# Kernel optimization log

Measured on AMD Instinct MI355X. Metric: run time of the kernel, lower is better.

## Reference

```python
import jax, jax.numpy as jnp
import numpy as np

B, T, E, H = 8, 1024, 768, 12  # batch, num_tokens, embed_dim (=dk=dv), num_heads


def setup_inputs() -> dict:
    key = jax.random.key(0)
    ks = jax.random.split(key, 5)
    return {
        "x": jax.random.normal(ks[0], (B, T, E), dtype=jnp.float32),
        "WQ": jax.random.normal(ks[1], (H, E, E), dtype=jnp.float32),
        "WK": jax.random.normal(ks[2], (H, E, E), dtype=jnp.float32),
        "WV": jax.random.normal(ks[3], (H, E, E), dtype=jnp.float32),
        "WO": jax.random.normal(ks[4], (H * E, E), dtype=jnp.float32),
    }


def reference(x, WQ, WK, WV, WO):
    b, t, e = x.shape
    h = WQ.shape[0]
    dk = WQ.shape[2]
    dv = WV.shape[2]
    # Batched QKV projections for all heads at once: (h, b, t, d)
    Q = jnp.einsum('bte,hek->hbtk', x, WQ)
    K = jnp.einsum('bte,hek->hbtk', x, WK)
    V = jnp.einsum('bte,hev->hbtv', x, WV)
    # Faithful quirk: original does K.view(b, e, t) -- a row-major RESHAPE,
    # not a transpose (valid because dk == e).
    K_rs = K.reshape(h, b, e, t)
    scores = jnp.matmul(Q, K_rs)  # (h, b, t, t)
    # Faithful quirks: scale by sqrt(num_tokens) (K.size(1) == t), and
    # Softmax(1) normalizes over the QUERY axis (axis 1 of (b,t,t) -> axis -2).
    A = jax.nn.softmax(scores / jnp.sqrt(jnp.asarray(t, scores.dtype)), axis=-2)
    Z = jnp.matmul(A, V)  # (h, b, t, dv)
    # Original: Z[bb] has layout (h, t, dv); reshape(t, h*dv) flat in row-major.
    Zc = jnp.transpose(Z, (1, 0, 2, 3)).reshape(b, h, t, dv)
    Zc = Zc.reshape(b, h * t * dv).reshape(b, t, h * dv)  # row-major flat of (h,t,dv)
    return jnp.matmul(Zc, WO)  # (b, t, e)
```

## Files before the change

kernel.cpp:

```cpp
#include <hip/hip_runtime.h>


typedef __bf16 bf16x8 __attribute__((ext_vector_type(8)));
typedef float  f32x4  __attribute__((ext_vector_type(4)));
typedef unsigned short u16;
typedef u16 u16x8 __attribute__((ext_vector_type(8)));
typedef u16 u16x4 __attribute__((ext_vector_type(4)));
typedef unsigned int u32;

#define RC 16

__device__ __forceinline__ float bf2f(u16 u) {
    union { u32 i; float f; } x; x.i = ((u32)u) << 16; return x.f;
}
__device__ __forceinline__ u16 f2bf(float f) {
    __bf16 h = (__bf16)f; union { __bf16 b; u16 u; } x; x.b = h; return x.u;
}
__device__ __forceinline__ void split2(float v, u16& h, u16& l) {
    h = f2bf(v); l = f2bf(v - bf2f(h));
}

__device__ __forceinline__ void gl16(const void* g, void* l) {
    __builtin_amdgcn_global_load_lds(
        (const __attribute__((address_space(1))) u32*)g,
        (__attribute__((address_space(3))) u32*)l, 16, 0, 0);
}

template<int BKMAJ, int WIN>
__device__ __forceinline__ void core(
    const u16* __restrict__ Ah, const u16* __restrict__ Al,
    const u16* __restrict__ Bh, const u16* __restrict__ Bl,
    float* __restrict__ C, u16* __restrict__ Ch, u16* __restrict__ Cl,
    int K, int lda, int ldb, int ldc,
    long long aShift, long long aHi, const u16* __restrict__ zp,
    int mClip, int mode, int mtile, int kChunk, int kChunks, int n0)
{
    __shared__ u16 Ahs[4096], Als[4096], Bhs[4096], Bls[4096];

    const int tid = threadIdx.x, lane = tid & 63, w = tid >> 6;
    const int m0 = mtile * 128;
    const int wm = (w & 1) << 6, wn = (w >> 1) << 6;
    const int lr = lane & 15, lq = lane >> 4;
    const int rs = (lr >> 1) & 3;
    const int fro = (lq ^ rs) << 4;

    const int srow = (w << 4) + (lane >> 2);
    const int kk = (((lane & 3) ^ ((srow >> 1) & 3)) << 3);
    const int lds0 = (w << 10), lds1 = lds0 + 4096;

    const int nB = tid & 127, khB = (tid >> 7) << 4;
    const int rsB = (nB >> 1) & 3;
    const int sB0 = (((khB >> 3) ^ rsB) << 4);
    const int sB1 = ((((khB >> 3) | 1) ^ rsB) << 4);

    f32x4 acc[4][4] = {};
    const int kLen = K / kChunks;
    const int kBeg = kChunk * kLen, kEnd = kBeg + kLen;

    u16 rBh[16], rBl[16];
    auto loadB = [&](int k0) {
        if constexpr (BKMAJ) {
#pragma unroll
            for (int j = 0; j < 16; ++j) {
                long long o = (long long)(k0 + khB + j) * ldb + n0 + nB;
                rBh[j] = Bh[o]; rBl[j] = Bl[o];
            }
        }
    };
    auto stage = [&](int k0) {
        long long o1 = (long long)(m0 + srow) * lda + k0 + kk;
        long long o2 = o1 + (long long)64 * lda;
        const u16 *p1h = Ah + o1, *p1l = Al + o1;
        const u16 *p2h = Ah + o2, *p2l = Al + o2;
        if constexpr (WIN) {
            long long a1 = o1 + aShift, a2 = o2 + aShift;
            bool v1 = (a1 >= 0) && (a1 < aHi);
            bool v2 = (a2 >= 0) && (a2 < aHi);
            p1h = v1 ? Ah + a1 : zp;  p1l = v1 ? Al + a1 : zp;
            p2h = v2 ? Ah + a2 : zp;  p2l = v2 ? Al + a2 : zp;
        }
        gl16(p1h, (char*)Ahs + lds0);  gl16(p2h, (char*)Ahs + lds1);
        gl16(p1l, (char*)Als + lds0);  gl16(p2l, (char*)Als + lds1);
        if constexpr (!BKMAJ) {
            long long b1 = (long long)(n0 + srow) * ldb + k0 + kk;
            long long b2 = b1 + (long long)64 * ldb;
            gl16(Bh + b1, (char*)Bhs + lds0);  gl16(Bh + b2, (char*)Bhs + lds1);
            gl16(Bl + b1, (char*)Bls + lds0);  gl16(Bl + b2, (char*)Bls + lds1);
        }
    };
    auto writeB = [&]() {
        if constexpr (BKMAJ) {
            u16x8 h0, h1, l0, l1;
#pragma unroll
            for (int j = 0; j < 8; ++j) {
                h0[j] = rBh[j]; h1[j] = rBh[j + 8];
                l0[j] = rBl[j]; l1[j] = rBl[j + 8];
            }
            *(u16x8*)((char*)Bhs + nB * 64 + sB0) = h0;
            *(u16x8*)((char*)Bhs + nB * 64 + sB1) = h1;
            *(u16x8*)((char*)Bls + nB * 64 + sB0) = l0;
            *(u16x8*)((char*)Bls + nB * 64 + sB1) = l1;
        }
    };

    loadB(kBeg);
    for (int k0 = kBeg; k0 < kEnd; k0 += 32) {
        stage(k0);
        writeB();
        __syncthreads();
        if (k0 + 32 < kEnd) loadB(k0 + 32);

        bf16x8 a_h[4], a_l[4];
#pragma unroll
        for (int mi = 0; mi < 4; ++mi) {
            int off = ((wm + (mi << 4) + lr) << 6) + fro;
            a_h[mi] = *(const bf16x8*)((char*)Ahs + off);
            a_l[mi] = *(const bf16x8*)((char*)Als + off);
        }
#pragma unroll
        for (int ni = 0; ni < 4; ++ni) {
            int off = ((wn + (ni << 4) + lr) << 6) + fro;
            bf16x8 b_h = *(const bf16x8*)((char*)Bhs + off);
            bf16x8 b_l = *(const bf16x8*)((char*)Bls + off);
#pragma unroll
            for (int mi = 0; mi < 4; ++mi) {
                acc[mi][ni] = __builtin_amdgcn_mfma_f32_16x16x32_bf16(a_h[mi], b_h, acc[mi][ni], 0, 0, 0);
                acc[mi][ni] = __builtin_amdgcn_mfma_f32_16x16x32_bf16(a_l[mi], b_h, acc[mi][ni], 0, 0, 0);
                acc[mi][ni] = __builtin_amdgcn_mfma_f32_16x16x32_bf16(a_h[mi], b_l, acc[mi][ni], 0, 0, 0);
            }
        }
        __syncthreads();
    }

#pragma unroll
    for (int mi = 0; mi < 4; ++mi)
#pragma unroll
        for (int r = 0; r < 4; ++r) {
            int row = m0 + wm + (mi << 4) + (lq << 2) + r;
            if (row < mClip) {
#pragma unroll
                for (int ni = 0; ni < 4; ++ni) {
                    long long off = (long long)row * ldc + n0 + wn + (ni << 4) + lr;
                    float v = acc[mi][ni][r];
                    if (mode == 2)      atomicAdd(&C[off], v);
                    else if (mode == 1) { u16 hh, ll; split2(v, hh, ll); Ch[off] = hh; Cl[off] = ll; }
                    else                C[off] = v;
                }
            }
        }
}

__global__ __launch_bounds__(256, 3)
void g_qkv(const u16* __restrict__ Xh, const u16* __restrict__ Xl,
           const u16* __restrict__ Wth, const u16* __restrict__ Wtl,
           u16* __restrict__ Qh, u16* __restrict__ Ql,
           u16* __restrict__ Kh, u16* __restrict__ Kl,
           u16* __restrict__ Vh, u16* __restrict__ Vl)
{
    const long long EE = 768LL * 768;
    int z = blockIdx.z;
    const u16* bh = Wth + (long long)z * EE;
    const u16* bl = Wtl + (long long)z * EE;
    u16* ch = (z == 0) ? Qh : (z == 1) ? Kh : Vh;
    u16* cl = (z == 0) ? Ql : (z == 1) ? Kl : Vl;
    core<0, 0>(Xh, Xl, bh, bl, nullptr, ch, cl, 768, 768, 768, 768,
               0, 0, nullptr, 1 << 30, 1, blockIdx.y, 0, 1, blockIdx.x * 128);
}

__global__ __launch_bounds__(256, 3)
void g_km(const u16* __restrict__ Ah, const u16* __restrict__ Al,
          const u16* __restrict__ Bh, const u16* __restrict__ Bl,
          u16* __restrict__ Ch, u16* __restrict__ Cl,
          int K, int lda, int ldb, int ldc,
          long long sA, long long sB, long long sC)
{
    long long z = blockIdx.z;
    core<1, 0>(Ah + z * sA, Al + z * sA, Bh + z * sB, Bl + z * sB,
               nullptr, Ch + z * sC, Cl + z * sC,
               K, lda, ldb, ldc, 0, 0, nullptr, 1 << 30, 1,
               blockIdx.y, 0, 1, blockIdx.x * 128);
}

__global__ __launch_bounds__(256, 3)
void g_fin(const u16* __restrict__ Zh, const u16* __restrict__ Zl,
           const u16* __restrict__ WOth, const u16* __restrict__ WOtl,
           float* __restrict__ C, const u16* __restrict__ zp,
           long long aShift, int mClip, int kChunks)
{
    const long long TE_ = 786432;
    long long z = blockIdx.z;
    core<0, 1>(Zh + z * TE_, Zl + z * TE_, WOth, WOtl, C + z * TE_,
               nullptr, nullptr, 9216, 9216, 9216, 768,
               aShift, TE_, zp, mClip, 2, 0, blockIdx.y, kChunks, blockIdx.x * 128);
}

__global__ void k_split(const float* __restrict__ s, u16* __restrict__ h,
                        u16* __restrict__ l, long long n)
{
    long long i = ((long long)blockIdx.x * blockDim.x + threadIdx.x) * 4;
    long long stride = (long long)gridDim.x * blockDim.x * 4;
    for (; i < n; i += stride) {
        float4 v = *(const float4*)(s + i);
        u16x4 hh, ll;
        u16 h0, l0, h1, l1, h2, l2, h3, l3;
        split2(v.x, h0, l0); split2(v.y, h1, l1);
        split2(v.z, h2, l2); split2(v.w, h3, l3);
        hh[0] = h0; hh[1] = h1; hh[2] = h2; hh[3] = h3;
        ll[0] = l0; ll[1] = l1; ll[2] = l2; ll[3] = l3;
        *(u16x4*)(h + i) = hh;
        *(u16x4*)(l + i) = ll;
    }
}

__global__ void k_tsplit(const float* __restrict__ s, u16* __restrict__ dh,
                         u16* __restrict__ dl, int Ks, int Ns)
{
    __shared__ float t[32][33];
    int tx = threadIdx.x & 31, ty = threadIdx.x >> 5;
    int kb = blockIdx.y << 5, nb_ = blockIdx.x << 5;
#pragma unroll
    for (int i = 0; i < 4; ++i)
        t[ty + 8 * i][tx] = s[(long long)(kb + ty + 8 * i) * Ns + nb_ + tx];
    __syncthreads();
#pragma unroll
    for (int i = 0; i < 4; ++i) {
        float v = t[tx][ty + 8 * i];
        long long o = (long long)(nb_ + ty + 8 * i) * Ks + kb + tx;
        u16 hh, ll; split2(v, hh, ll);
        dh[o] = hh; dl[o] = ll;
    }
}

__global__ void k_tsplit3(const float* __restrict__ s0, const float* __restrict__ s1,
                          const float* __restrict__ s2,
                          u16* __restrict__ dh, u16* __restrict__ dl)
{
    const int E = 768; const long long EE = (long long)E * E;
    const float* s = (blockIdx.z == 0) ? s0 : (blockIdx.z == 1) ? s1 : s2;
    u16* h = dh + blockIdx.z * EE;
    u16* l = dl + blockIdx.z * EE;
    __shared__ float t[32][33];
    int tx = threadIdx.x & 31, ty = threadIdx.x >> 5;
    int kb = blockIdx.y << 5, nb_ = blockIdx.x << 5;
#pragma unroll
    for (int i = 0; i < 4; ++i)
        t[ty + 8 * i][tx] = s[(long long)(kb + ty + 8 * i) * E + nb_ + tx];
    __syncthreads();
#pragma unroll
    for (int i = 0; i < 4; ++i) {
        float v = t[tx][ty + 8 * i];
        long long o = (long long)(nb_ + ty + 8 * i) * E + kb + tx;
        u16 hh, ll; split2(v, hh, ll);
        h[o] = hh; l[o] = ll;
    }
}

__global__ __launch_bounds__(256)
void sm_part(const u16* __restrict__ Sh, const u16* __restrict__ Sl,
             float2* __restrict__ part, int T, float scale)
{
    const int lane = threadIdx.x & 63, seg = threadIdx.x >> 6;
    const int j0 = blockIdx.x * 256 + lane * 4;
    const long long base = (long long)blockIdx.z * T * T;
    const int rpc = T / RC, rps = rpc / 4;
    const int r0 = blockIdx.y * rpc + seg * rps;

    float m[4] = {-3.4e38f, -3.4e38f, -3.4e38f, -3.4e38f};
    float s[4] = {0.f, 0.f, 0.f, 0.f};
    for (int r = 0; r < rps; ++r) {
        long long o = base + (long long)(r0 + r) * T + j0;
        u16x4 vh = *(const u16x4*)(Sh + o);
        u16x4 vl = *(const u16x4*)(Sl + o);
#pragma unroll
        for (int c = 0; c < 4; ++c) {
            float v = (bf2f(vh[c]) + bf2f(vl[c])) * scale;
            float mn = fmaxf(m[c], v);
            s[c] = s[c] * __expf(m[c] - mn) + __expf(v - mn);
            m[c] = mn;
        }
    }
    __shared__ float4 smm[4][64], sss[4][64];
    smm[seg][lane] = make_float4(m[0], m[1], m[2], m[3]);
    sss[seg][lane] = make_float4(s[0], s[1], s[2], s[3]);
    __syncthreads();
    if (seg == 0) {
#pragma unroll
        for (int q = 1; q < 4; ++q) {
            float4 mq4 = smm[q][lane], sq4 = sss[q][lane];
            float mq[4] = {mq4.x, mq4.y, mq4.z, mq4.w};
            float sq[4] = {sq4.x, sq4.y, sq4.z, sq4.w};
#pragma unroll
            for (int c = 0; c < 4; ++c) {
                float mn = fmaxf(m[c], mq[c]);
                s[c] = s[c] * __expf(m[c] - mn) + sq[c] * __expf(mq[c] - mn);
                m[c] = mn;
            }
        }
        long long pb = ((long long)blockIdx.z * RC + blockIdx.y) * T + j0;
#pragma unroll
        for (int c = 0; c < 4; ++c)
            part[pb + c] = make_float2(m[c], s[c]);
    }
}

__global__ __launch_bounds__(256)
void sm_fin2(const float2* __restrict__ part, float2* __restrict__ fin, int T)
{
    int j = blockIdx.x * 256 + threadIdx.x;
    long long pb = (long long)blockIdx.y * RC * T + j;
    float mt = -3.4e38f, st = 0.f;
#pragma unroll
    for (int q = 0; q < RC; ++q) {
        float2 p = part[pb + (long long)q * T];
        float mn = fmaxf(mt, p.x);
        st = st * __expf(mt - mn) + p.y * __expf(p.x - mn);
        mt = mn;
    }
    fin[(long long)blockIdx.y * T + j] = make_float2(mt, 1.f / st);
}

__global__ __launch_bounds__(256)
void sm_norm(u16* __restrict__ Sh, u16* __restrict__ Sl,
             const float2* __restrict__ fin, int T, float scale)
{
    const int lane = threadIdx.x & 63, seg = threadIdx.x >> 6;
    const int j0 = blockIdx.x * 256 + lane * 4;
    const long long base = (long long)blockIdx.z * T * T;
    const int rpc = T / RC, rps = rpc / 4;
    const int r0 = blockIdx.y * rpc + seg * rps;
    float mt[4], inv[4];
#pragma unroll
    for (int c = 0; c < 4; ++c) {
        float2 f = fin[(long long)blockIdx.z * T + j0 + c];
        mt[c] = f.x; inv[c] = f.y;
    }
    for (int r = 0; r < rps; ++r) {
        long long o = base + (long long)(r0 + r) * T + j0;
        u16x4 vh = *(const u16x4*)(Sh + o);
        u16x4 vl = *(const u16x4*)(Sl + o);
        u16x4 oh, ol;
#pragma unroll
        for (int c = 0; c < 4; ++c) {
            float v = (bf2f(vh[c]) + bf2f(vl[c])) * scale;
            float p = __expf(v - mt[c]) * inv[c];
            u16 hh, ll; split2(p, hh, ll);
            oh[c] = hh; ol[c] = ll;
        }
        *(u16x4*)(Sh + o) = oh;
        *(u16x4*)(Sl + o) = ol;
    }
}

extern "C" void kernel_launch(void* const* d_in, const int* in_sizes, int n_in,
                              void* d_out, int out_size, void* d_ws, size_t ws_size,
                              hipStream_t stream)
{
    const float* x  = (const float*)d_in[0];
    const float* WQ = (const float*)d_in[1];
    const float* WK = (const float*)d_in[2];
    const float* WV = (const float*)d_in[3];
    const float* WO = (const float*)d_in[4];
    float* out = (float*)d_out;

    const int B = 8, T = 1024, E = 768, H = 12;
    const long long TE = (long long)T * E;
    const long long TT = (long long)T * T;
    const long long HE = (long long)H * E;
    const long long EE = (long long)E * E;

    char* p = (char*)d_ws;
    u16* Xh   = (u16*)p; p += (size_t)B * TE * 2;
    u16* Xl   = (u16*)p; p += (size_t)B * TE * 2;
    u16* WOth = (u16*)p; p += (size_t)E * HE * 2;
    u16* WOtl = (u16*)p; p += (size_t)E * HE * 2;
    u16* Wth  = (u16*)p; p += (size_t)3 * EE * 2;
    u16* Wtl  = (u16*)p; p += (size_t)3 * EE * 2;
    u16* zp   = (u16*)p; p += 4096;
    float2* part = (float2*)p; p += (size_t)B * RC * T * sizeof(float2);
    float2* finb = (float2*)p; p += (size_t)B * T * sizeof(float2);
    size_t used = (size_t)(p - (char*)d_ws);
    size_t slice = (size_t)(6 * TE + 2 * TT) * 2;
    int NC = (int)((ws_size - used) / slice);
    if (NC < 1) NC = 1;
    if (NC > B) NC = B;
    u16* Qh = (u16*)p; p += (size_t)NC * TE * 2;
    u16* Ql = (u16*)p; p += (size_t)NC * TE * 2;
    u16* Kh = (u16*)p; p += (size_t)NC * TE * 2;
    u16* Kl = (u16*)p; p += (size_t)NC * TE * 2;
    u16* Vh = (u16*)p; p += (size_t)NC * TE * 2;
    u16* Vl = (u16*)p; p += (size_t)NC * TE * 2;
    u16* Sh = (u16*)p; p += (size_t)NC * TT * 2;
    u16* Sl = (u16*)p; p += (size_t)NC * TT * 2;
    u16* Zh = Qh;
    u16* Zl = Ql;

    hipMemsetAsync(out, 0, (size_t)B * TE * sizeof(float), stream);
    hipMemsetAsync(zp, 0, 4096, stream);

    dim3 blk(256);

    k_split<<<2048, blk, 0, stream>>>(x, Xh, Xl, (long long)B * TE);
    k_tsplit<<<dim3(E / 32, (int)HE / 32), blk, 0, stream>>>(WO, WOth, WOtl, (int)HE, E);

    for (int h = 0; h < H; ++h) {
        const int i_lo = (int)(((long long)h * TE) / HE);
        const long long aShift = (long long)i_lo * HE - (long long)h * TE;

        k_tsplit3<<<dim3(24, 24, 3), blk, 0, stream>>>(
            WQ + (size_t)h * EE, WK + (size_t)h * EE, WV + (size_t)h * EE, Wth, Wtl);

        for (int b0 = 0; b0 < B; b0 += NC) {
            const int nb = (B - b0 < NC) ? (B - b0) : NC;

            g_qkv<<<dim3(6, nb * T / 128, 3), blk, 0, stream>>>(
                Xh + (size_t)b0 * TE, Xl + (size_t)b0 * TE, Wth, Wtl,
                Qh, Ql, Kh, Kl, Vh, Vl);

            g_km<<<dim3(8, 8, nb), blk, 0, stream>>>(
                Qh, Ql, Kh, Kl, Sh, Sl, 768, 768, 1024, 1024, TE, TE, TT);

            sm_part<<<dim3(T / 256, RC, nb), blk, 0, stream>>>(Sh, Sl, part, T, 0.03125f);
            sm_fin2<<<dim3(T / 256, nb), blk, 0, stream>>>(part, finb, T);
            sm_norm<<<dim3(T / 256, RC, nb), blk, 0, stream>>>(Sh, Sl, finb, T, 0.03125f);

            g_km<<<dim3(6, 8, nb), blk, 0, stream>>>(
                Sh, Sl, Vh, Vl, Zh, Zl, 1024, 1024, 768, 768, TT, TE, TE);

            g_fin<<<dim3(6, 24, nb), blk, 0, stream>>>(
                Zh, Zl, WOth, WOtl,
                out + (size_t)b0 * TE + (size_t)i_lo * E, zp,
                aShift, T - i_lo, 24);
        }
    }
}
```

Measured before the change: 4.289 ms.

## Pre-transpose K and V so all GEMMs use async LDS loads

Adds a tiled transpose kernel that writes K and V in N-major layout. All batched GEMMs can then use the global_load_lds staging path, replacing the old K-major B path that did scalar register loads and LDS writes. The price is two extra transpose passes per head and chunk plus extra workspace for the transposed K. Launch bounds are also raised to 4 blocks per CU, and the QKV grid folds the weight index into blockIdx.x.

New measurement: 4.340 ms. No clear change (+1.2%).

```diff
diff --git a/kernel.cpp b/kernel.cpp
--- a/kernel.cpp
+++ b/kernel.cpp
@@ -4,7 +4,7 @@
 typedef __bf16 bf16x8 __attribute__((ext_vector_type(8)));
 typedef float  f32x4  __attribute__((ext_vector_type(4)));
 typedef unsigned short u16;
-typedef u16 u16x8 __attribute__((ext_vector_type(8)));
+typedef u16 u16x2 __attribute__((ext_vector_type(2)));
 typedef u16 u16x4 __attribute__((ext_vector_type(4)));
 typedef unsigned int u32;
 
@@ -26,7 +26,7 @@
         (__attribute__((address_space(3))) u32*)l, 16, 0, 0);
 }
 
-template<int BKMAJ, int WIN>
+template<int WIN>
 __device__ __forceinline__ void core(
     const u16* __restrict__ Ah, const u16* __restrict__ Al,
     const u16* __restrict__ Bh, const u16* __restrict__ Bl,
@@ -48,25 +48,10 @@
     const int kk = (((lane & 3) ^ ((srow >> 1) & 3)) << 3);
     const int lds0 = (w << 10), lds1 = lds0 + 4096;
 
-    const int nB = tid & 127, khB = (tid >> 7) << 4;
-    const int rsB = (nB >> 1) & 3;
-    const int sB0 = (((khB >> 3) ^ rsB) << 4);
-    const int sB1 = ((((khB >> 3) | 1) ^ rsB) << 4);
-
     f32x4 acc[4][4] = {};
     const int kLen = K / kChunks;
     const int kBeg = kChunk * kLen, kEnd = kBeg + kLen;
 
-    u16 rBh[16], rBl[16];
-    auto loadB = [&](int k0) {
-        if constexpr (BKMAJ) {
-#pragma unroll
-            for (int j = 0; j < 16; ++j) {
-                long long o = (long long)(k0 + khB + j) * ldb + n0 + nB;
-                rBh[j] = Bh[o]; rBl[j] = Bl[o];
-            }
-        }
-    };
     auto stage = [&](int k0) {
         long long o1 = (long long)(m0 + srow) * lda + k0 + kk;
         long long o2 = o1 + (long long)64 * lda;
@@ -81,34 +66,15 @@
         }
         gl16(p1h, (char*)Ahs + lds0);  gl16(p2h, (char*)Ahs + lds1);
         gl16(p1l, (char*)Als + lds0);  gl16(p2l, (char*)Als + lds1);
-        if constexpr (!BKMAJ) {
-            long long b1 = (long long)(n0 + srow) * ldb + k0 + kk;
-            long long b2 = b1 + (long long)64 * ldb;
-            gl16(Bh + b1, (char*)Bhs + lds0);  gl16(Bh + b2, (char*)Bhs + lds1);
-            gl16(Bl + b1, (char*)Bls + lds0);  gl16(Bl + b2, (char*)Bls + lds1);
-        }
+        long long b1 = (long long)(n0 + srow) * ldb + k0 + kk;
+        long long b2 = b1 + (long long)64 * ldb;
+        gl16(Bh + b1, (char*)Bhs + lds0);  gl16(Bh + b2, (char*)Bhs + lds1);
+        gl16(Bl + b1, (char*)Bls + lds0);  gl16(Bl + b2, (char*)Bls + lds1);
     };
-    auto writeB = [&]() {
-        if constexpr (BKMAJ) {
-            u16x8 h0, h1, l0, l1;
-#pragma unroll
-            for (int j = 0; j < 8; ++j) {
-                h0[j] = rBh[j]; h1[j] = rBh[j + 8];
-                l0[j] = rBl[j]; l1[j] = rBl[j + 8];
-            }
-            *(u16x8*)((char*)Bhs + nB * 64 + sB0) = h0;
-            *(u16x8*)((char*)Bhs + nB * 64 + sB1) = h1;
-            *(u16x8*)((char*)Bls + nB * 64 + sB0) = l0;
-            *(u16x8*)((char*)Bls + nB * 64 + sB1) = l1;
-        }
-    };
-
-    loadB(kBeg);
+
     for (int k0 = kBeg; k0 < kEnd; k0 += 32) {
         stage(k0);
-        writeB();
         __syncthreads();
-        if (k0 + 32 < kEnd) loadB(k0 + 32);
 
         bf16x8 a_h[4], a_l[4];
 #pragma unroll
@@ -150,7 +116,7 @@
         }
 }
 
-__global__ __launch_bounds__(256, 3)
+__global__ __launch_bounds__(256, 4)
 void g_qkv(const u16* __restrict__ Xh, const u16* __restrict__ Xl,
            const u16* __restrict__ Wth, const u16* __restrict__ Wtl,
            u16* __restrict__ Qh, u16* __restrict__ Ql,
@@ -158,30 +124,31 @@
            u16* __restrict__ Vh, u16* __restrict__ Vl)
 {
     const long long EE = 768LL * 768;
-    int z = blockIdx.z;
+    int z  = blockIdx.x % 3;
+    int n0 = (blockIdx.x / 3) * 128;
     const u16* bh = Wth + (long long)z * EE;
     const u16* bl = Wtl + (long long)z * EE;
     u16* ch = (z == 0) ? Qh : (z == 1) ? Kh : Vh;
     u16* cl = (z == 0) ? Ql : (z == 1) ? Kl : Vl;
-    core<0, 0>(Xh, Xl, bh, bl, nullptr, ch, cl, 768, 768, 768, 768,
-               0, 0, nullptr, 1 << 30, 1, blockIdx.y, 0, 1, blockIdx.x * 128);
-}
-
-__global__ __launch_bounds__(256, 3)
-void g_km(const u16* __restrict__ Ah, const u16* __restrict__ Al,
+    core<0>(Xh, Xl, bh, bl, nullptr, ch, cl, 768, 768, 768, 768,
+            0, 0, nullptr, 1 << 30, 1, blockIdx.y, 0, 1, n0);
+}
+
+__global__ __launch_bounds__(256, 4)
+void g_bt(const u16* __restrict__ Ah, const u16* __restrict__ Al,
           const u16* __restrict__ Bh, const u16* __restrict__ Bl,
           u16* __restrict__ Ch, u16* __restrict__ Cl,
           int K, int lda, int ldb, int ldc,
           long long sA, long long sB, long long sC)
 {
     long long z = blockIdx.z;
-    core<1, 0>(Ah + z * sA, Al + z * sA, Bh + z * sB, Bl + z * sB,
-               nullptr, Ch + z * sC, Cl + z * sC,
-               K, lda, ldb, ldc, 0, 0, nullptr, 1 << 30, 1,
-               blockIdx.y, 0, 1, blockIdx.x * 128);
-}
-
-__global__ __launch_bounds__(256, 3)
+    core<0>(Ah + z * sA, Al + z * sA, Bh + z * sB, Bl + z * sB,
+            nullptr, Ch + z * sC, Cl + z * sC,
+            K, lda, ldb, ldc, 0, 0, nullptr, 1 << 30, 1,
+            blockIdx.y, 0, 1, blockIdx.x * 128);
+}
+
+__global__ __launch_bounds__(256, 4)
 void g_fin(const u16* __restrict__ Zh, const u16* __restrict__ Zl,
            const u16* __restrict__ WOth, const u16* __restrict__ WOtl,
            float* __restrict__ C, const u16* __restrict__ zp,
@@ -189,9 +156,43 @@
 {
     const long long TE_ = 786432;
     long long z = blockIdx.z;
-    core<0, 1>(Zh + z * TE_, Zl + z * TE_, WOth, WOtl, C + z * TE_,
-               nullptr, nullptr, 9216, 9216, 9216, 768,
-               aShift, TE_, zp, mClip, 2, 0, blockIdx.y, kChunks, blockIdx.x * 128);
+    core<1>(Zh + z * TE_, Zl + z * TE_, WOth, WOtl, C + z * TE_,
+            nullptr, nullptr, 9216, 9216, 9216, 768,
+            aShift, TE_, zp, mClip, 2, 0, blockIdx.y, kChunks, blockIdx.x * 128);
+}
+
+__global__ __launch_bounds__(256)
+void t_hl(const u16* __restrict__ ih, const u16* __restrict__ il,
+          u16* __restrict__ oh, u16* __restrict__ ol, int R, int C)
+{
+    long long zo = (long long)blockIdx.z * R * C;
+    __shared__ u16 L[64][34];
+    const int t = threadIdx.x, tx = t & 31, ty = t >> 5;
+    const int r0 = blockIdx.y * 32, c0 = blockIdx.x * 64;
+    const int orow = t >> 2;
+
+    const u16* iv[2] = { ih + zo, il + zo };
+    u16* ov[2] = { oh + zo, ol + zo };
+#pragma unroll
+    for (int p = 0; p < 2; ++p) {
+        const u16* in = iv[p];  u16* out = ov[p];
+#pragma unroll
+        for (int i = 0; i < 4; ++i) {
+            u16x2 v = *(const u16x2*)&in[(long long)(r0 + ty + 8 * i) * C + c0 + tx * 2];
+            L[tx * 2][ty + 8 * i] = v[0];
+            L[tx * 2 + 1][ty + 8 * i] = v[1];
+        }
+        __syncthreads();
+#pragma unroll
+        for (int i = 0; i < 4; ++i) {
+            int j = (t & 3) * 4 + i;
+            u16x2 wv;
+            wv[0] = L[orow][j * 2];
+            wv[1] = L[orow][j * 2 + 1];
+            *(u16x2*)&out[(long long)(c0 + orow) * R + r0 + j * 2] = wv;
+        }
+        __syncthreads();
+    }
 }
 
 __global__ void k_split(const float* __restrict__ s, u16* __restrict__ h,
@@ -379,20 +380,24 @@
     float2* part = (float2*)p; p += (size_t)B * RC * T * sizeof(float2);
     float2* finb = (float2*)p; p += (size_t)B * T * sizeof(float2);
     size_t used = (size_t)(p - (char*)d_ws);
-    size_t slice = (size_t)(6 * TE + 2 * TT) * 2;
+    size_t slice = (size_t)(8 * TE + 2 * TT) * 2;
     int NC = (int)((ws_size - used) / slice);
     if (NC < 1) NC = 1;
     if (NC > B) NC = B;
-    u16* Qh = (u16*)p; p += (size_t)NC * TE * 2;
-    u16* Ql = (u16*)p; p += (size_t)NC * TE * 2;
-    u16* Kh = (u16*)p; p += (size_t)NC * TE * 2;
-    u16* Kl = (u16*)p; p += (size_t)NC * TE * 2;
-    u16* Vh = (u16*)p; p += (size_t)NC * TE * 2;
-    u16* Vl = (u16*)p; p += (size_t)NC * TE * 2;
-    u16* Sh = (u16*)p; p += (size_t)NC * TT * 2;
-    u16* Sl = (u16*)p; p += (size_t)NC * TT * 2;
+    u16* Qh  = (u16*)p; p += (size_t)NC * TE * 2;
+    u16* Ql  = (u16*)p; p += (size_t)NC * TE * 2;
+    u16* Kh  = (u16*)p; p += (size_t)NC * TE * 2;
+    u16* Kl  = (u16*)p; p += (size_t)NC * TE * 2;
+    u16* Vh  = (u16*)p; p += (size_t)NC * TE * 2;
+    u16* Vl  = (u16*)p; p += (size_t)NC * TE * 2;
+    u16* Kth = (u16*)p; p += (size_t)NC * TE * 2;
+    u16* Ktl = (u16*)p; p += (size_t)NC * TE * 2;
+    u16* Sh  = (u16*)p; p += (size_t)NC * TT * 2;
+    u16* Sl  = (u16*)p; p += (size_t)NC * TT * 2;
     u16* Zh = Qh;
     u16* Zl = Ql;
+    u16* Vth = Kh;
+    u16* Vtl = Kl;
 
     hipMemsetAsync(out, 0, (size_t)B * TE * sizeof(float), stream);
     hipMemsetAsync(zp, 0, 4096, stream);
@@ -412,19 +417,22 @@
         for (int b0 = 0; b0 < B; b0 += NC) {
             const int nb = (B - b0 < NC) ? (B - b0) : NC;
 
-            g_qkv<<<dim3(6, nb * T / 128, 3), blk, 0, stream>>>(
+            g_qkv<<<dim3(18, nb * T / 128), blk, 0, stream>>>(
                 Xh + (size_t)b0 * TE, Xl + (size_t)b0 * TE, Wth, Wtl,
                 Qh, Ql, Kh, Kl, Vh, Vl);
 
-            g_km<<<dim3(8, 8, nb), blk, 0, stream>>>(
-                Qh, Ql, Kh, Kl, Sh, Sl, 768, 768, 1024, 1024, TE, TE, TT);
+            t_hl<<<dim3(16, 24, nb), blk, 0, stream>>>(Kh, Kl, Kth, Ktl, 768, 1024);
+            t_hl<<<dim3(12, 32, nb), blk, 0, stream>>>(Vh, Vl, Vth, Vtl, 1024, 768);
+
+            g_bt<<<dim3(8, 8, nb), blk, 0, stream>>>(
+                Qh, Ql, Kth, Ktl, Sh, Sl, 768, 768, 768, 1024, TE, TE, TT);
 
             sm_part<<<dim3(T / 256, RC, nb), blk, 0, stream>>>(Sh, Sl, part, T, 0.03125f);
             sm_fin2<<<dim3(T / 256, nb), blk, 0, stream>>>(part, finb, T);
             sm_norm<<<dim3(T / 256, RC, nb), blk, 0, stream>>>(Sh, Sl, finb, T, 0.03125f);
 
-            g_km<<<dim3(6, 8, nb), blk, 0, stream>>>(
-                Sh, Sl, Vh, Vl, Zh, Zl, 1024, 1024, 768, 768, TT, TE, TE);
+            g_bt<<<dim3(6, 8, nb), blk, 0, stream>>>(
+                Sh, Sl, Vth, Vtl, Zh, Zl, 1024, 1024, 1024, 768, TT, TE, TE);
 
             g_fin<<<dim3(6, 24, nb), blk, 0, stream>>>(
                 Zh, Zl, WOth, WOtl,
```

## Pre-split all head weights once and defer output projection to single batched GEMM

Applied to the files above, without the earlier changes.

Splits and transposes all 36 QKV weight matrices into bf16 hi/lo once up front instead of per head, and swaps the loop order to batch-outer/head-inner. When workspace allows, each head's Z is kept in a full Z buffer and the output projection runs as one split-K GEMM per batch chunk, replacing twelve per-head atomic-accumulating launches. g_qkv folds the Q/K/V selector into blockIdx.x, and launch bounds are raised to 4 waves per SIMD. The cost is a larger workspace footprint, plus a fallback path whose g_fin grid changes from 24 to 12 y-blocks and kChunks.

Measured after the change: 7.543 ms. 1.76x slower.

```diff
diff --git a/kernel.cpp b/kernel.cpp
--- a/kernel.cpp
+++ b/kernel.cpp
@@ -150,7 +150,7 @@
         }
 }
 
-__global__ __launch_bounds__(256, 3)
+__global__ __launch_bounds__(256, 4)
 void g_qkv(const u16* __restrict__ Xh, const u16* __restrict__ Xl,
            const u16* __restrict__ Wth, const u16* __restrict__ Wtl,
            u16* __restrict__ Qh, u16* __restrict__ Ql,
@@ -158,13 +158,14 @@
            u16* __restrict__ Vh, u16* __restrict__ Vl)
 {
     const long long EE = 768LL * 768;
-    int z = blockIdx.z;
+    int z  = blockIdx.x % 3;
+    int n0 = (blockIdx.x / 3) * 128;
     const u16* bh = Wth + (long long)z * EE;
     const u16* bl = Wtl + (long long)z * EE;
     u16* ch = (z == 0) ? Qh : (z == 1) ? Kh : Vh;
     u16* cl = (z == 0) ? Ql : (z == 1) ? Kl : Vl;
     core<0, 0>(Xh, Xl, bh, bl, nullptr, ch, cl, 768, 768, 768, 768,
-               0, 0, nullptr, 1 << 30, 1, blockIdx.y, 0, 1, blockIdx.x * 128);
+               0, 0, nullptr, 1 << 30, 1, blockIdx.y, 0, 1, n0);
 }
 
 __global__ __launch_bounds__(256, 3)
@@ -179,6 +180,20 @@
                nullptr, Ch + z * sC, Cl + z * sC,
                K, lda, ldb, ldc, 0, 0, nullptr, 1 << 30, 1,
                blockIdx.y, 0, 1, blockIdx.x * 128);
+}
+
+__global__ __launch_bounds__(256, 4)
+void g_out(const u16* __restrict__ Zh, const u16* __restrict__ Zl,
+           const u16* __restrict__ WOth, const u16* __restrict__ WOtl,
+           float* __restrict__ C, int kChunks)
+{
+    const long long ZB = 12LL * 786432;
+    long long z = blockIdx.z;
+    int mtile = blockIdx.y / kChunks;
+    int kc    = blockIdx.y % kChunks;
+    core<0, 0>(Zh + z * ZB, Zl + z * ZB, WOth, WOtl, C + z * 786432LL,
+               nullptr, nullptr, 9216, 9216, 9216, 768,
+               0, 0, nullptr, 1 << 30, 2, mtile, kc, kChunks, blockIdx.x * 128);
 }
 
 __global__ __launch_bounds__(256, 3)
@@ -255,6 +270,31 @@
     }
 }
 
+__global__ void k_tsplitA(const float* __restrict__ WQ, const float* __restrict__ WK,
+                          const float* __restrict__ WV,
+                          u16* __restrict__ dh, u16* __restrict__ dl)
+{
+    const int E = 768; const long long EE = (long long)E * E;
+    int hz = blockIdx.z, hh_ = hz / 3, w = hz % 3;
+    const float* s = ((w == 0) ? WQ : (w == 1) ? WK : WV) + (long long)hh_ * EE;
+    u16* h = dh + (long long)hz * EE;
+    u16* l = dl + (long long)hz * EE;
+    __shared__ float t[32][33];
+    int tx = threadIdx.x & 31, ty = threadIdx.x >> 5;
+    int kb = blockIdx.y << 5, nb_ = blockIdx.x << 5;
+#pragma unroll
+    for (int i = 0; i < 4; ++i)
+        t[ty + 8 * i][tx] = s[(long long)(kb + ty + 8 * i) * E + nb_ + tx];
+    __syncthreads();
+#pragma unroll
+    for (int i = 0; i < 4; ++i) {
+        float v = t[tx][ty + 8 * i];
+        long long o = (long long)(nb_ + ty + 8 * i) * E + kb + tx;
+        u16 hh, ll; split2(v, hh, ll);
+        h[o] = hh; l[o] = ll;
+    }
+}
+
 __global__ __launch_bounds__(256)
 void sm_part(const u16* __restrict__ Sh, const u16* __restrict__ Sl,
              float2* __restrict__ part, int T, float scale)
@@ -373,16 +413,32 @@
     u16* Xl   = (u16*)p; p += (size_t)B * TE * 2;
     u16* WOth = (u16*)p; p += (size_t)E * HE * 2;
     u16* WOtl = (u16*)p; p += (size_t)E * HE * 2;
-    u16* Wth  = (u16*)p; p += (size_t)3 * EE * 2;
-    u16* Wtl  = (u16*)p; p += (size_t)3 * EE * 2;
     u16* zp   = (u16*)p; p += 4096;
     float2* part = (float2*)p; p += (size_t)B * RC * T * sizeof(float2);
     float2* finb = (float2*)p; p += (size_t)B * T * sizeof(float2);
-    size_t used = (size_t)(p - (char*)d_ws);
-    size_t slice = (size_t)(6 * TE + 2 * TT) * 2;
-    int NC = (int)((ws_size - used) / slice);
-    if (NC < 1) NC = 1;
+    size_t used0 = (size_t)(p - (char*)d_ws);
+
+    const size_t slice = (size_t)(6 * TE + 2 * TT) * 2;
+    const size_t zsl   = (size_t)12 * TE * 4;
+    const size_t wt12  = (size_t)36 * EE * 2 * 2;
+    const size_t wt1   = (size_t)3 * EE * 2 * 2;
+
+    long long avail = (long long)ws_size - (long long)used0;
+    bool wtAll = false, tierA = false;
+    int NC = 0;
+    long long nca = (avail - (long long)wt12) / (long long)(slice + zsl);
+    if (nca >= 2) { tierA = true; wtAll = true; NC = (int)(nca > 8 ? 8 : nca); }
+    else if (avail >= (long long)(wt12 + 8 * slice)) { wtAll = true; NC = 8; }
+    else if (avail >= (long long)(wt1 + 8 * slice))  { NC = 8; }
+    else {
+        NC = (int)((avail - (long long)wt1) / (long long)slice);
+        if (NC < 1) NC = 1;
+    }
     if (NC > B) NC = B;
+
+    u16* Wth = (u16*)p;  u16* Wtl;
+    if (wtAll) { Wtl = Wth + (size_t)36 * EE; p += wt12; }
+    else       { Wtl = Wth + (size_t)3 * EE;  p += wt1;  }
     u16* Qh = (u16*)p; p += (size_t)NC * TE * 2;
     u16* Ql = (u16*)p; p += (size_t)NC * TE * 2;
     u16* Kh = (u16*)p; p += (size_t)NC * TE * 2;
@@ -391,6 +447,8 @@
     u16* Vl = (u16*)p; p += (size_t)NC * TE * 2;
     u16* Sh = (u16*)p; p += (size_t)NC * TT * 2;
     u16* Sl = (u16*)p; p += (size_t)NC * TT * 2;
+    u16* Zallh = (u16*)p; if (tierA) p += (size_t)NC * 12 * TE * 2;
+    u16* Zalll = (u16*)p;
     u16* Zh = Qh;
     u16* Zl = Ql;
 
@@ -401,19 +459,24 @@
 
     k_split<<<2048, blk, 0, stream>>>(x, Xh, Xl, (long long)B * TE);
     k_tsplit<<<dim3(E / 32, (int)HE / 32), blk, 0, stream>>>(WO, WOth, WOtl, (int)HE, E);
-
-    for (int h = 0; h < H; ++h) {
-        const int i_lo = (int)(((long long)h * TE) / HE);
-        const long long aShift = (long long)i_lo * HE - (long long)h * TE;
-
-        k_tsplit3<<<dim3(24, 24, 3), blk, 0, stream>>>(
-            WQ + (size_t)h * EE, WK + (size_t)h * EE, WV + (size_t)h * EE, Wth, Wtl);
-
-        for (int b0 = 0; b0 < B; b0 += NC) {
-            const int nb = (B - b0 < NC) ? (B - b0) : NC;
-
-            g_qkv<<<dim3(6, nb * T / 128, 3), blk, 0, stream>>>(
-                Xh + (size_t)b0 * TE, Xl + (size_t)b0 * TE, Wth, Wtl,
+    if (wtAll)
+        k_tsplitA<<<dim3(24, 24, 36), blk, 0, stream>>>(WQ, WK, WV, Wth, Wtl);
+
+    for (int b0 = 0; b0 < B; b0 += NC) {
+        const int nb = (B - b0 < NC) ? (B - b0) : NC;
+
+        for (int h = 0; h < H; ++h) {
+            const u16* wh; const u16* wl;
+            if (wtAll) { wh = Wth + (size_t)h * 3 * EE; wl = Wtl + (size_t)h * 3 * EE; }
+            else {
+                k_tsplit3<<<dim3(24, 24, 3), blk, 0, stream>>>(
+                    WQ + (size_t)h * EE, WK + (size_t)h * EE, WV + (size_t)h * EE,
+                    Wth, Wtl);
+                wh = Wth; wl = Wtl;
+            }
+
+            g_qkv<<<dim3(18, nb * T / 128), blk, 0, stream>>>(
+                Xh + (size_t)b0 * TE, Xl + (size_t)b0 * TE, wh, wl,
                 Qh, Ql, Kh, Kl, Vh, Vl);
 
             g_km<<<dim3(8, 8, nb), blk, 0, stream>>>(
@@ -423,13 +486,26 @@
             sm_fin2<<<dim3(T / 256, nb), blk, 0, stream>>>(part, finb, T);
             sm_norm<<<dim3(T / 256, RC, nb), blk, 0, stream>>>(Sh, Sl, finb, T, 0.03125f);
 
-            g_km<<<dim3(6, 8, nb), blk, 0, stream>>>(
-                Sh, Sl, Vh, Vl, Zh, Zl, 1024, 1024, 768, 768, TT, TE, TE);
-
-            g_fin<<<dim3(6, 24, nb), blk, 0, stream>>>(
-                Zh, Zl, WOth, WOtl,
-                out + (size_t)b0 * TE + (size_t)i_lo * E, zp,
-                aShift, T - i_lo, 24);
-        }
-    }
-}
+            if (tierA) {
+                g_km<<<dim3(6, 8, nb), blk, 0, stream>>>(
+                    Sh, Sl, Vh, Vl,
+                    Zallh + (size_t)h * TE, Zalll + (size_t)h * TE,
+                    1024, 1024, 768, 768, TT, TE, 12 * TE);
+            } else {
+                const int i_lo = (int)(((long long)h * TE) / HE);
+                const long long aShift = (long long)i_lo * HE - (long long)h * TE;
+                g_km<<<dim3(6, 8, nb), blk, 0, stream>>>(
+                    Sh, Sl, Vh, Vl, Zh, Zl, 1024, 1024, 768, 768, TT, TE, TE);
+                g_fin<<<dim3(6, 12, nb), blk, 0, stream>>>(
+                    Zh, Zl, WOth, WOtl,
+                    out + (size_t)b0 * TE + (size_t)i_lo * E, zp,
+                    aShift, T - i_lo, 12);
+            }
+        }
+
+        if (tierA) {
+            g_out<<<dim3(6, 8 * 4, nb), blk, 0, stream>>>(
+                Zallh, Zalll, WOth, WOtl, out + (size_t)b0 * TE, 4);
+        }
+    }
+}
```
